# Kernel optimization log

Measured on AMD Instinct MI355X. Metric: run time of the kernel, lower is better.

The kernel has to match this reference:

```python
import jax, jax.numpy as jnp
import numpy as np

N_NODES = 50000
N_EDGES = 800000
N_GRAPHS = 64
EPS = 1e-12


def setup_inputs() -> dict:
    key = jax.random.key(0)
    ks = jax.random.split(key, 8)
    x = jax.random.normal(ks[0], (N_NODES, 128), dtype=jnp.float32)
    edge_index = jax.random.randint(ks[1], (2, N_EDGES), 0, N_NODES, dtype=jnp.int64)
    batch = jnp.sort(jax.random.randint(ks[2], (N_NODES,), 0, N_GRAPHS, dtype=jnp.int64))
    W1 = jax.random.normal(ks[3], (128, 64), dtype=jnp.float32) * 0.1
    W2 = jax.random.normal(ks[4], (64, 64), dtype=jnp.float32) * 0.1
    W3 = jax.random.normal(ks[5], (64, 64), dtype=jnp.float32) * 0.1
    Wl = jax.random.normal(ks[6], (128, 32), dtype=jnp.float32) * 0.1
    return {
        'x': x, 'edge_index': edge_index, 'batch': batch,
        'W1': W1, 'b1': jnp.zeros((64,), jnp.float32),
        'W2': W2, 'b2': jnp.zeros((64,), jnp.float32),
        'W3': W3, 'b3': jnpp if False else jnp.zeros((64,), jnp.float32),
        'Wl': Wl, 'bl': jnp.zeros((32,), jnp.float32),
    }


def _gcn_conv(h, W, b, src, dst, dinv, enorm, n):
    # PyG GCNConv: D^-1/2 (A+I) D^-1/2 (h W) + b, self-loops included analytically
    hw = h @ W
    agg = jax.ops.segment_sum(hw[src] * enorm[:, None], dst, num_segments=n)
    agg = agg + (dinv * dinv)[:, None] * hw  # self-loop term
    return agg + b


def _norm_relu(h):
    # F.normalize(p=2, dim=1) then relu
    nrm = jnp.sqrt(jnp.sum(h * h, axis=1, keepdims=True))
    return jax.nn.relu(h / jnp.maximum(nrm, EPS))


def reference(x, edge_index, batch, W1, b1, W2, b2, W3, b3, Wl, bl):
    n = x.shape[0]
    src, dst = edge_index[0], edge_index[1]
    # degree with self-loops (counts incoming edges at target, +1 for self-loop)
    deg = jax.ops.segment_sum(jnp.ones((src.shape[0],), x.dtype), dst, num_segments=n) + 1.0
    dinv = 1.0 / jnp.sqrt(deg)
    enorm = dinv[src] * dinv[dst]

    h = _norm_relu(_gcn_conv(x, W1, b1, src, dst, dinv, enorm, n))
    h = _norm_relu(_gcn_conv(h, W2, b2, src, dst, dinv, enorm, n))
    h = _norm_relu(_gcn_conv(h, W3, b3, src, dst, dinv, enorm, n))

    counts = jax.ops.segment_sum(jnp.ones((n,), x.dtype), batch, num_segments=N_GRAPHS)
    x_mean = jax.ops.segment_sum(h, batch, num_segments=N_GRAPHS) / jnp.maximum(counts, 1.0)[:, None]
    x_max = jax.ops.segment_max(h, batch, num_segments=N_GRAPHS)
    x_max = jnp.where(counts[:, None] > 0, x_max, 0.0)  # guard empty graphs

    pooled = jnp.concatenate([x_mean, x_max], axis=-1)  # [B, 2*hidden]
    return pooled @ Wl + bl
```

## Files before the change

### kernel.cpp

```cpp
#include <hip/hip_runtime.h>
#include <hip/hip_bf16.h>

#define N_NODES 50000
#define N_EDGES 800000
#define N_GRAPHS 64
#define HID 64
#define SCAN_NB 196
#define FILL_RANGES 8
#define RANGE_SIZE ((N_NODES + FILL_RANGES - 1) / FILL_RANGES)
#define MM1_BLOCKS ((N_NODES + 63) / 64)
#define FILL_BLOCKS (FILL_RANGES * ((N_EDGES + 255) / 256))

static inline size_t align256(size_t x) { return (x + 255) & ~(size_t)255; }

typedef __attribute__((ext_vector_type(8))) short short8v;
typedef __attribute__((ext_vector_type(4))) float f32x4;

__device__ __forceinline__ unsigned short f2bf(float f) {
    unsigned int u = __float_as_uint(f);
    unsigned int r = (u + 0x7fffu + ((u >> 16) & 1u)) >> 16;
    return (unsigned short)r;
}
__device__ __forceinline__ float bf2f(unsigned short h) {
    return __uint_as_float(((unsigned int)h) << 16);
}

__global__ void zero2(int* __restrict__ a, int na, int* __restrict__ b, int nb) {
    int i = blockIdx.x * blockDim.x + threadIdx.x;
    if (i < na) a[i] = 0;
    else if (i < na + nb) b[i - na] = 0;
}

__global__ void deg_kernel(const int* __restrict__ ei, int* __restrict__ cnt) {
    int e = blockIdx.x * blockDim.x + threadIdx.x;
    if (e < N_EDGES) atomicAdd(&cnt[ei[N_EDGES + e]], 1);
}

__global__ __launch_bounds__(256) void scan_a(const int* __restrict__ cnt,
                                              int* __restrict__ incl,
                                              int* __restrict__ bsum) {
    __shared__ int sd[256];
    int t = threadIdx.x;
    int i = blockIdx.x * 256 + t;
    int v = (i < N_NODES) ? cnt[i] : 0;
    sd[t] = v;
    __syncthreads();
    for (int off = 1; off < 256; off <<= 1) {
        int u = (t >= off) ? sd[t - off] : 0;
        __syncthreads();
        sd[t] += u;
        __syncthreads();
    }
    if (i < N_NODES) incl[i] = sd[t];
    if (t == 255) bsum[blockIdx.x] = sd[255];
}

__global__ __launch_bounds__(384) void scan_b_gstart(const int* __restrict__ bsum,
                                                     int* __restrict__ boff,
                                                     const int* __restrict__ batch,
                                                     int* __restrict__ gstart) {
    __shared__ int sd[256];
    int t = threadIdx.x;
    int v = 0;
    if (t < 256) {
        v = (t < SCAN_NB) ? bsum[t] : 0;
        sd[t] = v;
    }
    __syncthreads();
    for (int off = 1; off < 256; off <<= 1) {
        int u = (t < 256 && t >= off) ? sd[t - off] : 0;
        __syncthreads();
        if (t < 256) sd[t] += u;
        __syncthreads();
    }
    if (t < SCAN_NB) boff[t] = sd[t] - v;
    if (t >= 256 && t - 256 <= N_GRAPHS) {
        int g = t - 256;
        int lo = 0, hi = N_NODES;
        while (lo < hi) {
            int mid = (lo + hi) >> 1;
            if (batch[mid] < g) lo = mid + 1; else hi = mid;
        }
        gstart[g] = lo;
    }
}

__global__ void scan_c(const int* __restrict__ cnt, const int* __restrict__ incl,
                       const int* __restrict__ boff, int* __restrict__ row_ptr,
                       int* __restrict__ fill_ptr, float* __restrict__ dinv) {
    int i = blockIdx.x * blockDim.x + threadIdx.x;
    if (i < N_NODES) {
        int c = cnt[i];
        int run = boff[i >> 8] + incl[i];
        row_ptr[i + 1] = run;
        fill_ptr[i] = run - c;
        dinv[i] = rsqrtf((float)c + 1.0f);
        if (i == 0) row_ptr[0] = 0;
    }
}

__global__ __launch_bounds__(256) void fill_mm1_kernel(const int* __restrict__ ei,
                                                       int* __restrict__ fill_ptr,
                                                       int* __restrict__ csr_src,
                                                       const float* __restrict__ h,
                                                       const float* __restrict__ W,
                                                       const float* __restrict__ dinv,
                                                       unsigned short* __restrict__ hw2) {
    constexpr int K = 128;
    constexpr int NSTEP = K / 32;
    __shared__ unsigned short sWH[NSTEP * 4 * 64 * 8];
    __shared__ unsigned short sWL[NSTEP * 4 * 64 * 8];
    int tid = threadIdx.x;

    if (blockIdx.x >= MM1_BLOCKS) {
        int fb = blockIdx.x - MM1_BLOCKS;
        int r = fb & (FILL_RANGES - 1);
        int e = (fb >> 3) * 256 + tid;
        if (e >= N_EDGES) return;
        int dst = ei[N_EDGES + e];
        int lo = r * RANGE_SIZE;
        if (dst >= lo && dst < lo + RANGE_SIZE) {
            int src = ei[e];
            int pos = atomicAdd(&fill_ptr[dst], 1);
            csr_src[pos] = src;
        }
        return;
    }

    int r0 = blockIdx.x * 64;
#pragma unroll 1
    for (int ent = tid; ent < NSTEP * 4 * 64; ent += 256) {
        int lane_e = ent & 63;
        int c = (ent >> 6) & 3;
        int step = ent >> 8;
        int kb = step * 32 + (lane_e >> 4) * 8;
        int n = c * 16 + (lane_e & 15);
#pragma unroll
        for (int j = 0; j < 8; ++j) {
            float f = W[(kb + j) * 64 + n];
            unsigned short hi = f2bf(f);
            sWH[ent * 8 + j] = hi;
            sWL[ent * 8 + j] = f2bf(f - bf2f(hi));
        }
    }
    __syncthreads();

    int lane = tid & 63;
    int wid = tid >> 6;
    int arow = min(r0 + wid * 16 + (lane & 15), N_NODES - 1);
    const float* ap = h + (size_t)arow * K;
    int klane = (lane >> 4) * 8;

    f32x4 acc[4];
#pragma unroll
    for (int c = 0; c < 4; ++c) acc[c] = (f32x4){0.f, 0.f, 0.f, 0.f};

#pragma unroll 1
    for (int step = 0; step < NSTEP; ++step) {
        int kb = step * 32 + klane;
        float4 f0 = *(const float4*)&ap[kb];
        float4 f1 = *(const float4*)&ap[kb + 4];
        float fv[8] = {f0.x, f0.y, f0.z, f0.w, f1.x, f1.y, f1.z, f1.w};
        short8v ahi, alo;
#pragma unroll
        for (int j = 0; j < 8; ++j) {
            unsigned short hi = f2bf(fv[j]);
            ahi[j] = (short)hi;
            alo[j] = (short)f2bf(fv[j] - bf2f(hi));
        }
#pragma unroll
        for (int c = 0; c < 4; ++c) {
            short8v bh = *(const short8v*)&sWH[((step * 4 + c) * 64 + lane) * 8];
            short8v bl = *(const short8v*)&sWL[((step * 4 + c) * 64 + lane) * 8];
            acc[c] = __builtin_amdgcn_mfma_f32_16x16x32_bf16(ahi, bh, acc[c], 0, 0, 0);
            acc[c] = __builtin_amdgcn_mfma_f32_16x16x32_bf16(alo, bh, acc[c], 0, 0, 0);
            acc[c] = __builtin_amdgcn_mfma_f32_16x16x32_bf16(ahi, bl, acc[c], 0, 0, 0);
        }
    }

    int rb = r0 + wid * 16 + (lane >> 4) * 4;
#pragma unroll
    for (int j = 0; j < 4; ++j) {
        int row = rb + j;
        if (row < N_NODES) {
            float dv = dinv[row];
#pragma unroll
            for (int c = 0; c < 4; ++c) {
                hw2[(size_t)row * 64 + c * 16 + (lane & 15)] = f2bf(dv * acc[c][j]);
            }
        }
    }
}

template <int K>
__global__ __launch_bounds__(256) void mfma_matmul(const float* __restrict__ h,
                                                   const float* __restrict__ W,
                                                   const float* __restrict__ dinv,
                                                   unsigned short* __restrict__ hw2) {
    constexpr int NSTEP = K / 32;
    __shared__ unsigned short sWH[NSTEP * 4 * 64 * 8];
    __shared__ unsigned short sWL[NSTEP * 4 * 64 * 8];
    int tid = threadIdx.x;
    int r0 = blockIdx.x * 64;

#pragma unroll 1
    for (int ent = tid; ent < NSTEP * 4 * 64; ent += 256) {
        int lane_e = ent & 63;
        int c = (ent >> 6) & 3;
        int step = ent >> 8;
        int kb = step * 32 + (lane_e >> 4) * 8;
        int n = c * 16 + (lane_e & 15);
#pragma unroll
        for (int j = 0; j < 8; ++j) {
            float f = W[(kb + j) * 64 + n];
            unsigned short hi = f2bf(f);
            sWH[ent * 8 + j] = hi;
            sWL[ent * 8 + j] = f2bf(f - bf2f(hi));
        }
    }
    __syncthreads();

    int lane = tid & 63;
    int wid = tid >> 6;
    int arow = min(r0 + wid * 16 + (lane & 15), N_NODES - 1);
    const float* ap = h + (size_t)arow * K;
    int klane = (lane >> 4) * 8;

    f32x4 acc[4];
#pragma unroll
    for (int c = 0; c < 4; ++c) acc[c] = (f32x4){0.f, 0.f, 0.f, 0.f};

#pragma unroll 1
    for (int step = 0; step < NSTEP; ++step) {
        int kb = step * 32 + klane;
        float4 f0 = *(const float4*)&ap[kb];
        float4 f1 = *(const float4*)&ap[kb + 4];
        float fv[8] = {f0.x, f0.y, f0.z, f0.w, f1.x, f1.y, f1.z, f1.w};
        short8v ahi, alo;
#pragma unroll
        for (int j = 0; j < 8; ++j) {
            unsigned short hi = f2bf(fv[j]);
            ahi[j] = (short)hi;
            alo[j] = (short)f2bf(fv[j] - bf2f(hi));
        }
#pragma unroll
        for (int c = 0; c < 4; ++c) {
            short8v bh = *(const short8v*)&sWH[((step * 4 + c) * 64 + lane) * 8];
            short8v bl = *(const short8v*)&sWL[((step * 4 + c) * 64 + lane) * 8];
            acc[c] = __builtin_amdgcn_mfma_f32_16x16x32_bf16(ahi, bh, acc[c], 0, 0, 0);
            acc[c] = __builtin_amdgcn_mfma_f32_16x16x32_bf16(alo, bh, acc[c], 0, 0, 0);
            acc[c] = __builtin_amdgcn_mfma_f32_16x16x32_bf16(ahi, bl, acc[c], 0, 0, 0);
        }
    }

    int rb = r0 + wid * 16 + (lane >> 4) * 4;
#pragma unroll
    for (int j = 0; j < 4; ++j) {
        int row = rb + j;
        if (row < N_NODES) {
            float dv = dinv[row];
#pragma unroll
            for (int c = 0; c < 4; ++c) {
                hw2[(size_t)row * 64 + c * 16 + (lane & 15)] = f2bf(dv * acc[c][j]);
            }
        }
    }
}

template <bool POOL>
__global__ __launch_bounds__(256) void agg_kernel(const unsigned short* __restrict__ hw2,
                                                  const int* __restrict__ row_ptr,
                                                  const int* __restrict__ csr_src,
                                                  const float* __restrict__ dinv,
                                                  const float* __restrict__ b,
                                                  float* __restrict__ hout,
                                                  const int* __restrict__ batch,
                                                  float* __restrict__ gsum,
                                                  float* __restrict__ gmax) {
    __shared__ float sh[4][64];
    int tid = threadIdx.x;
    int node = blockIdx.x * 4 + (tid >> 6);
    int lane = tid & 63;
    int grp = lane >> 3;
    int gl  = lane & 7;
    int s = row_ptr[node], e = row_ptr[node + 1];

    float acc[8] = {0.f, 0.f, 0.f, 0.f, 0.f, 0.f, 0.f, 0.f};
    for (int base = s; base < e; base += 64) {
        int nE = min(64, e - base);
        int msrc = (lane < nE) ? csr_src[base + lane] : 0;
#pragma unroll
        for (int rr = 0; rr < 8; ++rr) {
            int i = rr * 8;
            if (i >= nE) break;
            int myi = i + grp;
            int src = __shfl(msrc, myi, 64);
            bool ok = myi < nE;
            int srcx = ok ? src : node;
            short8v v = *(const short8v*)&hw2[(size_t)srcx * 64 + gl * 8];
            if (ok) {
#pragma unroll
                for (int j = 0; j < 8; ++j) acc[j] += bf2f((unsigned short)v[j]);
            }
        }
    }
#pragma unroll
    for (int off = 8; off <= 32; off <<= 1) {
#pragma unroll
        for (int j = 0; j < 8; ++j) acc[j] += __shfl_xor(acc[j], off, 64);
    }
    short8v sv = *(const short8v*)&hw2[(size_t)node * 64 + gl * 8];
#pragma unroll
    for (int j = 0; j < 8; ++j) acc[j] += bf2f((unsigned short)sv[j]);

    float di = dinv[node];
    float4 b0 = *(const float4*)&b[gl * 8];
    float4 b1 = *(const float4*)&b[gl * 8 + 4];
    float val[8];
    val[0] = di * acc[0] + b0.x;
    val[1] = di * acc[1] + b0.y;
    val[2] = di * acc[2] + b0.z;
    val[3] = di * acc[3] + b0.w;
    val[4] = di * acc[4] + b1.x;
    val[5] = di * acc[5] + b1.y;
    val[6] = di * acc[6] + b1.z;
    val[7] = di * acc[7] + b1.w;

    float sq = 0.f;
#pragma unroll
    for (int j = 0; j < 8; ++j) sq += val[j] * val[j];
#pragma unroll
    for (int off = 1; off <= 4; off <<= 1) sq += __shfl_xor(sq, off, 64);
    float inv = 1.0f / fmaxf(sqrtf(sq), 1e-12f);

    if (POOL) {
        if (grp == 0) {
            float4 r0, r1;
            r0.x = fmaxf(val[0] * inv, 0.f);
            r0.y = fmaxf(val[1] * inv, 0.f);
            r0.z = fmaxf(val[2] * inv, 0.f);
            r0.w = fmaxf(val[3] * inv, 0.f);
            r1.x = fmaxf(val[4] * inv, 0.f);
            r1.y = fmaxf(val[5] * inv, 0.f);
            r1.z = fmaxf(val[6] * inv, 0.f);
            r1.w = fmaxf(val[7] * inv, 0.f);
            *(float4*)&sh[tid >> 6][gl * 8] = r0;
            *(float4*)&sh[tid >> 6][gl * 8 + 4] = r1;
        }
        __syncthreads();
        if (tid < 64) {
            int nb = blockIdx.x * 4;
            int gcur = batch[nb];
            float runsum = 0.f, runmax = 0.f;
#pragma unroll
            for (int w = 0; w < 4; ++w) {
                int g = batch[nb + w];
                if (g != gcur) {
                    atomicAdd(&gsum[gcur * 64 + tid], runsum);
                    atomicMax((int*)&gmax[gcur * 64 + tid], __float_as_int(runmax));
                    runsum = 0.f; runmax = 0.f; gcur = g;
                }
                float v = sh[w][tid];
                runsum += v;
                runmax = fmaxf(runmax, v);
            }
            atomicAdd(&gsum[gcur * 64 + tid], runsum);
            atomicMax((int*)&gmax[gcur * 64 + tid], __float_as_int(runmax));
        }
    } else {
        if (grp == 0) {
            float4 r0, r1;
            r0.x = fmaxf(val[0] * inv, 0.f);
            r0.y = fmaxf(val[1] * inv, 0.f);
            r0.z = fmaxf(val[2] * inv, 0.f);
            r0.w = fmaxf(val[3] * inv, 0.f);
            r1.x = fmaxf(val[4] * inv, 0.f);
            r1.y = fmaxf(val[5] * inv, 0.f);
            r1.z = fmaxf(val[6] * inv, 0.f);
            r1.w = fmaxf(val[7] * inv, 0.f);
            *(float4*)&hout[(size_t)node * 64 + gl * 8] = r0;
            *(float4*)&hout[(size_t)node * 64 + gl * 8 + 4] = r1;
        }
    }
}

__global__ __launch_bounds__(128) void linear_kernel(const float* __restrict__ gsum,
                                                     const float* __restrict__ gmax,
                                                     const int* __restrict__ gstart,
                                                     const float* __restrict__ Wl,
                                                     const float* __restrict__ bl,
                                                     float* __restrict__ out) {
    int g = blockIdx.x;
    __shared__ float pooled[128];
    int t = threadIdx.x;
    if (t < 64) {
        int cnt = gstart[g + 1] - gstart[g];
        pooled[t] = gsum[g * 64 + t] / fmaxf((float)cnt, 1.0f);
    } else {
        pooled[t] = gmax[g * 64 + (t - 64)];
    }
    __syncthreads();
    if (t < 32) {
        float acc = bl[t];
#pragma unroll 8
        for (int k = 0; k < 128; ++k) acc += pooled[k] * Wl[k * 32 + t];
        out[g * 32 + t] = acc;
    }
}

extern "C" void kernel_launch(void* const* d_in, const int* in_sizes, int n_in,
                              void* d_out, int out_size, void* d_ws, size_t ws_size,
                              hipStream_t stream) {
    const float* x        = (const float*)d_in[0];
    const int*   ei       = (const int*)d_in[1];
    const int*   batch    = (const int*)d_in[2];
    const float* W1       = (const float*)d_in[3];
    const float* b1       = (const float*)d_in[4];
    const float* W2       = (const float*)d_in[5];
    const float* b2       = (const float*)d_in[6];
    const float* W3       = (const float*)d_in[7];
    const float* b3       = (const float*)d_in[8];
    const float* Wl       = (const float*)d_in[9];
    const float* bl       = (const float*)d_in[10];
    float* out = (float*)d_out;

    char* ws = (char*)d_ws;
    int*   cnt      = (int*)ws;                 ws += align256((size_t)N_NODES * 4);
    int*   incl     = (int*)ws;                 ws += align256((size_t)N_NODES * 4);
    int*   bsum     = (int*)ws;                 ws += align256((size_t)SCAN_NB * 4);
    int*   boff     = (int*)ws;                 ws += align256((size_t)SCAN_NB * 4);
    int*   row_ptr  = (int*)ws;                 ws += align256((size_t)(N_NODES + 1) * 4);
    int*   fill_ptr = (int*)ws;                 ws += align256((size_t)N_NODES * 4);
    float* dinv     = (float*)ws;               ws += align256((size_t)N_NODES * 4);
    int*   gstart   = (int*)ws;                 ws += align256((size_t)(N_GRAPHS + 1) * 4);
    float* gsum     = (float*)ws;               ws += align256((size_t)N_GRAPHS * 64 * 4);
    float* gmax     = (float*)ws;               ws += align256((size_t)N_GRAPHS * 64 * 4);
    int*   csr_src  = (int*)ws;                 ws += align256((size_t)N_EDGES * 4);
    unsigned short* hwb = (unsigned short*)ws;  ws += align256((size_t)N_NODES * 64 * 2);
    float* h1       = (float*)ws;               ws += align256((size_t)N_NODES * 64 * 4);
    float* h2       = (float*)ws;               ws += align256((size_t)N_NODES * 64 * 4);

    hipLaunchKernelGGL(zero2, dim3((N_NODES + 2 * N_GRAPHS * 64 + 255) / 256), dim3(256), 0,
                       stream, cnt, N_NODES, (int*)gsum, 2 * N_GRAPHS * 64);
    hipLaunchKernelGGL(deg_kernel, dim3((N_EDGES + 255) / 256), dim3(256), 0, stream, ei, cnt);
    hipLaunchKernelGGL(scan_a, dim3(SCAN_NB), dim3(256), 0, stream, cnt, incl, bsum);
    hipLaunchKernelGGL(scan_b_gstart, dim3(1), dim3(384), 0, stream, bsum, boff, batch, gstart);
    hipLaunchKernelGGL(scan_c, dim3(SCAN_NB), dim3(256), 0, stream,
                       cnt, incl, boff, row_ptr, fill_ptr, dinv);

    const int mm_grid = (N_NODES + 63) / 64;
    const int agg_grid = N_NODES / 4;

    hipLaunchKernelGGL(fill_mm1_kernel, dim3(MM1_BLOCKS + FILL_BLOCKS), dim3(256), 0, stream,
                       ei, fill_ptr, csr_src, x, W1, dinv, hwb);

    hipLaunchKernelGGL((agg_kernel<false>), dim3(agg_grid), dim3(256), 0, stream,
                       hwb, row_ptr, csr_src, dinv, b1, h1, batch, gsum, gmax);
    hipLaunchKernelGGL((mfma_matmul<64>), dim3(mm_grid), dim3(256), 0, stream, h1, W2, dinv, hwb);
    hipLaunchKernelGGL((agg_kernel<false>), dim3(agg_grid), dim3(256), 0, stream,
                       hwb, row_ptr, csr_src, dinv, b2, h2, batch, gsum, gmax);
    hipLaunchKernelGGL((mfma_matmul<64>), dim3(mm_grid), dim3(256), 0, stream, h2, W3, dinv, hwb);
    hipLaunchKernelGGL((agg_kernel<true>), dim3(agg_grid), dim3(256), 0, stream,
                       hwb, row_ptr, csr_src, dinv, b3, (float*)nullptr, batch, gsum, gmax);

    hipLaunchKernelGGL(linear_kernel, dim3(N_GRAPHS), dim3(128), 0, stream,
                       gsum, gmax, gstart, Wl, bl, out);
}
```

Measured before the change: 207.7 us.

## Fuse three-pass scan into single decoupled-lookback kernel and store CSR indices as uint16

Replaces the three scan kernels (block scan, block-sum scan plus gstart, finalize) with one kernel that uses decoupled lookback through global flags, aggregates and prefixes, and computes gstart in an extra block. This removes two launches and the intermediate incl/boff round trips. It also narrows csr_src to 16-bit, halving index traffic in the fill and aggregation kernels. Node ids go up to 49999, which fits in 16 bits. The lookback relies on forward progress between blocks and zeroes the flags through the extended zero2 range, which now depends on gsum, gmax and bflag being laid out contiguously.

After: 221.5 us. 1.07x slower.

```diff
diff --git a/kernel.cpp b/kernel.cpp
--- a/kernel.cpp
+++ b/kernel.cpp
@@ -36,12 +36,32 @@
     if (e < N_EDGES) atomicAdd(&cnt[ei[N_EDGES + e]], 1);
 }
 
-__global__ __launch_bounds__(256) void scan_a(const int* __restrict__ cnt,
-                                              int* __restrict__ incl,
-                                              int* __restrict__ bsum) {
+__global__ __launch_bounds__(256) void scan_fused(const int* __restrict__ cnt,
+                                                  int* __restrict__ row_ptr,
+                                                  int* __restrict__ fill_ptr,
+                                                  float* __restrict__ dinv,
+                                                  int* __restrict__ bagg,
+                                                  int* __restrict__ bpre,
+                                                  int* __restrict__ bflag,
+                                                  const int* __restrict__ batch,
+                                                  int* __restrict__ gstart) {
+    int b = blockIdx.x;
+    int t = threadIdx.x;
+    if (b == SCAN_NB) {
+        if (t <= N_GRAPHS) {
+            int g = t;
+            int lo = 0, hi = N_NODES;
+            while (lo < hi) {
+                int mid = (lo + hi) >> 1;
+                if (batch[mid] < g) lo = mid + 1; else hi = mid;
+            }
+            gstart[g] = lo;
+        }
+        return;
+    }
     __shared__ int sd[256];
-    int t = threadIdx.x;
-    int i = blockIdx.x * 256 + t;
+    __shared__ int s_exc;
+    int i = b * 256 + t;
     int v = (i < N_NODES) ? cnt[i] : 0;
     sd[t] = v;
     __syncthreads();
@@ -51,57 +71,47 @@
         sd[t] += u;
         __syncthreads();
     }
-    if (i < N_NODES) incl[i] = sd[t];
-    if (t == 255) bsum[blockIdx.x] = sd[255];
-}
-
-__global__ __launch_bounds__(384) void scan_b_gstart(const int* __restrict__ bsum,
-                                                     int* __restrict__ boff,
-                                                     const int* __restrict__ batch,
-                                                     int* __restrict__ gstart) {
-    __shared__ int sd[256];
-    int t = threadIdx.x;
-    int v = 0;
-    if (t < 256) {
-        v = (t < SCAN_NB) ? bsum[t] : 0;
-        sd[t] = v;
+    int incl = sd[t];
+    int total = sd[255];
+    if (t == 0) {
+        if (b == 0) {
+            bpre[0] = total;
+            __threadfence();
+            atomicExch(&bflag[0], 2);
+            s_exc = 0;
+        } else {
+            bagg[b] = total;
+            __threadfence();
+            atomicExch(&bflag[b], 1);
+            int run = 0;
+            int j = b - 1;
+            while (true) {
+                int f;
+                do { f = atomicAdd(&bflag[j], 0); } while (f == 0);
+                if (f == 2) { run += atomicAdd(&bpre[j], 0); break; }
+                run += atomicAdd(&bagg[j], 0);
+                --j;
+            }
+            bpre[b] = run + total;
+            __threadfence();
+            atomicExch(&bflag[b], 2);
+            s_exc = run;
+        }
     }
     __syncthreads();
-    for (int off = 1; off < 256; off <<= 1) {
-        int u = (t < 256 && t >= off) ? sd[t - off] : 0;
-        __syncthreads();
-        if (t < 256) sd[t] += u;
-        __syncthreads();
-    }
-    if (t < SCAN_NB) boff[t] = sd[t] - v;
-    if (t >= 256 && t - 256 <= N_GRAPHS) {
-        int g = t - 256;
-        int lo = 0, hi = N_NODES;
-        while (lo < hi) {
-            int mid = (lo + hi) >> 1;
-            if (batch[mid] < g) lo = mid + 1; else hi = mid;
-        }
-        gstart[g] = lo;
-    }
-}
-
-__global__ void scan_c(const int* __restrict__ cnt, const int* __restrict__ incl,
-                       const int* __restrict__ boff, int* __restrict__ row_ptr,
-                       int* __restrict__ fill_ptr, float* __restrict__ dinv) {
-    int i = blockIdx.x * blockDim.x + threadIdx.x;
+    int exc = s_exc;
     if (i < N_NODES) {
-        int c = cnt[i];
-        int run = boff[i >> 8] + incl[i];
+        int run = exc + incl;
         row_ptr[i + 1] = run;
-        fill_ptr[i] = run - c;
-        dinv[i] = rsqrtf((float)c + 1.0f);
+        fill_ptr[i] = run - v;
+        dinv[i] = rsqrtf((float)v + 1.0f);
         if (i == 0) row_ptr[0] = 0;
     }
 }
 
 __global__ __launch_bounds__(256) void fill_mm1_kernel(const int* __restrict__ ei,
                                                        int* __restrict__ fill_ptr,
-                                                       int* __restrict__ csr_src,
+                                                       unsigned short* __restrict__ csr_src,
                                                        const float* __restrict__ h,
                                                        const float* __restrict__ W,
                                                        const float* __restrict__ dinv,
@@ -122,7 +132,7 @@
         if (dst >= lo && dst < lo + RANGE_SIZE) {
             int src = ei[e];
             int pos = atomicAdd(&fill_ptr[dst], 1);
-            csr_src[pos] = src;
+            csr_src[pos] = (unsigned short)src;
         }
         return;
     }
@@ -270,7 +280,7 @@
 template <bool POOL>
 __global__ __launch_bounds__(256) void agg_kernel(const unsigned short* __restrict__ hw2,
                                                   const int* __restrict__ row_ptr,
-                                                  const int* __restrict__ csr_src,
+                                                  const unsigned short* __restrict__ csr_src,
                                                   const float* __restrict__ dinv,
                                                   const float* __restrict__ b,
                                                   float* __restrict__ hout,
@@ -288,7 +298,7 @@
     float acc[8] = {0.f, 0.f, 0.f, 0.f, 0.f, 0.f, 0.f, 0.f};
     for (int base = s; base < e; base += 64) {
         int nE = min(64, e - base);
-        int msrc = (lane < nE) ? csr_src[base + lane] : 0;
+        int msrc = (lane < nE) ? (int)csr_src[base + lane] : 0;
 #pragma unroll
         for (int rr = 0; rr < 8; ++rr) {
             int i = rr * 8;
@@ -426,27 +436,26 @@
 
     char* ws = (char*)d_ws;
     int*   cnt      = (int*)ws;                 ws += align256((size_t)N_NODES * 4);
-    int*   incl     = (int*)ws;                 ws += align256((size_t)N_NODES * 4);
-    int*   bsum     = (int*)ws;                 ws += align256((size_t)SCAN_NB * 4);
-    int*   boff     = (int*)ws;                 ws += align256((size_t)SCAN_NB * 4);
     int*   row_ptr  = (int*)ws;                 ws += align256((size_t)(N_NODES + 1) * 4);
     int*   fill_ptr = (int*)ws;                 ws += align256((size_t)N_NODES * 4);
     float* dinv     = (float*)ws;               ws += align256((size_t)N_NODES * 4);
     int*   gstart   = (int*)ws;                 ws += align256((size_t)(N_GRAPHS + 1) * 4);
-    float* gsum     = (float*)ws;               ws += align256((size_t)N_GRAPHS * 64 * 4);
-    float* gmax     = (float*)ws;               ws += align256((size_t)N_GRAPHS * 64 * 4);
-    int*   csr_src  = (int*)ws;                 ws += align256((size_t)N_EDGES * 4);
+    float* gsum     = (float*)ws;               ws += (size_t)N_GRAPHS * 64 * 4;
+    float* gmax     = (float*)ws;               ws += (size_t)N_GRAPHS * 64 * 4;
+    int*   bflag    = (int*)ws;                 ws += align256((size_t)SCAN_NB * 4);
+    int*   bagg     = (int*)ws;                 ws += align256((size_t)SCAN_NB * 4);
+    int*   bpre     = (int*)ws;                 ws += align256((size_t)SCAN_NB * 4);
+    unsigned short* csr_src = (unsigned short*)ws; ws += align256((size_t)N_EDGES * 2);
     unsigned short* hwb = (unsigned short*)ws;  ws += align256((size_t)N_NODES * 64 * 2);
     float* h1       = (float*)ws;               ws += align256((size_t)N_NODES * 64 * 4);
     float* h2       = (float*)ws;               ws += align256((size_t)N_NODES * 64 * 4);
 
-    hipLaunchKernelGGL(zero2, dim3((N_NODES + 2 * N_GRAPHS * 64 + 255) / 256), dim3(256), 0,
-                       stream, cnt, N_NODES, (int*)gsum, 2 * N_GRAPHS * 64);
+    const int nzero2 = 2 * N_GRAPHS * 64 + SCAN_NB;
+    hipLaunchKernelGGL(zero2, dim3((N_NODES + nzero2 + 255) / 256), dim3(256), 0,
+                       stream, cnt, N_NODES, (int*)gsum, nzero2);
     hipLaunchKernelGGL(deg_kernel, dim3((N_EDGES + 255) / 256), dim3(256), 0, stream, ei, cnt);
-    hipLaunchKernelGGL(scan_a, dim3(SCAN_NB), dim3(256), 0, stream, cnt, incl, bsum);
-    hipLaunchKernelGGL(scan_b_gstart, dim3(1), dim3(384), 0, stream, bsum, boff, batch, gstart);
-    hipLaunchKernelGGL(scan_c, dim3(SCAN_NB), dim3(256), 0, stream,
-                       cnt, incl, boff, row_ptr, fill_ptr, dinv);
+    hipLaunchKernelGGL(scan_fused, dim3(SCAN_NB + 1), dim3(256), 0, stream,
+                       cnt, row_ptr, fill_ptr, dinv, bagg, bpre, bflag, batch, gstart);
 
     const int mm_grid = (N_NODES + 63) / 64;
     const int agg_grid = N_NODES / 4;
```
